# Kernel tuning notes

Hardware: AMD Instinct MI355X
Metric: run time of the kernel (lower is better)

The kernel has to match this reference:

```python
import jax, jax.numpy as jnp
import numpy as np

N_QUBITS = 11
DIM = 2 ** N_QUBITS
GAIN = 2 ** 0.5
LRMUL = 1.0
W_MUL = GAIN * 5 ** (-0.5) * LRMUL  # use_wscale=True path


def _build_unitary(weight):
    """Overall circuit unitary. Per qubit q the circuit applies rx, ry, rz
    (left_to_right composition => Rz @ Ry @ Rx on that qubit's subspace).
    Gates on distinct qubits commute, so the sequential product of expanded
    gates equals the kron over qubits of the per-qubit composite 2x2 gate,
    with qubit 0 as the leftmost kron factor (matches gate_expand_1toN)."""
    w = (weight * W_MUL).reshape(N_QUBITS, 3)
    half = w / 2
    c = jnp.cos(half)
    s = jnp.sin(half)
    cx, sx = c[:, 0], s[:, 0]
    cy, sy = c[:, 1], s[:, 1]
    ez = jnp.exp(-1j * half[:, 2])  # e^{-i phi_z / 2}
    zeros = jnp.zeros_like(ez)
    # [n, 2, 2] gate stacks (complex64)
    rx = jnp.stack([jnp.stack([cx + 0j, -1j * sx], -1),
                    jnp.stack([-1j * sx, cx + 0j], -1)], -2)
    ry = jnp.stack([jnp.stack([cy + 0j, -sy + 0j], -1),
                    jnp.stack([sy + 0j, cy + 0j], -1)], -2)
    rz = jnp.stack([jnp.stack([ez, zeros], -1),
                    jnp.stack([zeros, jnp.conj(ez)], -1)], -2)
    g = rz @ ry @ rx  # [n, 2, 2] composite per-qubit gate
    U = g[0]
    for q in range(1, N_QUBITS):  # loop over fixed small n_qubits is fine
        U = jnp.kron(U, g[q])
    return U  # [DIM, DIM] complex64


def setup_inputs() -> dict:
    key = jax.random.key(0)
    kx, kw = jax.random.split(key)
    x = jax.random.normal(kx, (DIM, DIM), dtype=jnp.float32)
    weight = jax.random.uniform(kw, (N_QUBITS * 3,), dtype=jnp.float32,
                                minval=0.0, maxval=2.0 * np.pi)
    return {"x": x, "weight": weight}


def reference(x, weight):
    U = _build_unitary(weight)
    xc = x.astype(jnp.complex64)
    # queryQ_out = U @ x @ U^dagger
    return U @ xc @ jnp.conj(U).T
```

## Files before the change

### kernel.cpp

```cpp
#include <hip/hip_runtime.h>
#include <hip/hip_fp16.h>


#define DIM 2048
#define NQ 11

typedef float v2f __attribute__((ext_vector_type(2)));

__device__ __forceinline__ int swz(int j) { return j ^ ((j >> 5) & 31); }

__device__ __forceinline__ float2 cmul(float2 a, float2 b) {
    return make_float2(a.x * b.x - a.y * b.y, a.x * b.y + a.y * b.x);
}

__device__ __forceinline__ v2f pkmul_swap(v2f s, v2f g) {
    v2f d;
    asm("v_pk_mul_f32 %0, %1, %2 op_sel:[1,0] op_sel_hi:[0,1]"
        : "=v"(d) : "v"(s), "v"(g));
    return d;
}
__device__ __forceinline__ v2f pkfma(v2f s0, v2f s1, v2f c) {
    v2f d;
    asm("v_pk_fma_f32 %0, %1, %2, %3" : "=v"(d) : "v"(s0), "v"(s1), "v"(c));
    return d;
}
__device__ __forceinline__ v2f pkfma_swap(v2f s0, v2f s1, v2f c) {
    v2f d;
    asm("v_pk_fma_f32 %0, %1, %2, %3 op_sel:[1,0,0] op_sel_hi:[0,1,1]"
        : "=v"(d) : "v"(s0), "v"(s1), "v"(c));
    return d;
}

struct PkGate {
    v2f x00, y00, x01, y01, x10, y10, x11, y11;
};

__device__ __forceinline__ void make_gate(const float* __restrict__ w, int q,
                                          int conj, float2* out4) {
    const float WM = 0.632455532033675866f;
    float hx = 0.5f * WM * w[q * 3 + 0];
    float hy = 0.5f * WM * w[q * 3 + 1];
    float hz = 0.5f * WM * w[q * 3 + 2];
    float cx, sx, cy, sy, cz, sz;
    sincosf(hx, &sx, &cx);
    sincosf(hy, &sy, &cy);
    sincosf(hz, &sz, &cz);
    float2 m00 = make_float2(cy * cx,  sy * sx);
    float2 m01 = make_float2(-sy * cx, -cy * sx);
    float2 m10 = make_float2(sy * cx,  -cy * sx);
    float2 m11 = make_float2(cy * cx,  -sy * sx);
    float2 ez  = make_float2(cz, -sz);
    float2 ezc = make_float2(cz,  sz);
    float2 g00 = cmul(ez, m00);
    float2 g01 = cmul(ez, m01);
    float2 g10 = cmul(ezc, m10);
    float2 g11 = cmul(ezc, m11);
    float sgn = conj ? -1.f : 1.f;
    out4[0] = make_float2(g00.x, sgn * g00.y);
    out4[1] = make_float2(g01.x, sgn * g01.y);
    out4[2] = make_float2(g10.x, sgn * g10.y);
    out4[3] = make_float2(g11.x, sgn * g11.y);
}

__device__ __forceinline__ void build_pk_gates(const float* __restrict__ wt,
                                               int t, int conj,
                                               v2f (*gsh)[8]) {
    if (t < NQ) {
        float2 e[4];
        make_gate(wt, t, conj, e);
#pragma unroll
        for (int k = 0; k < 4; ++k) {
            v2f px = {e[k].x, e[k].x};
            v2f py = {-e[k].y, e[k].y};
            gsh[t][2 * k + 0] = px;
            gsh[t][2 * k + 1] = py;
        }
    }
}

__device__ __forceinline__ void load_pkgate(const v2f (*gsh)[8], int q,
                                            PkGate& G) {
    G.x00 = gsh[q][0]; G.y00 = gsh[q][1];
    G.x01 = gsh[q][2]; G.y01 = gsh[q][3];
    G.x10 = gsh[q][4]; G.y10 = gsh[q][5];
    G.x11 = gsh[q][6]; G.y11 = gsh[q][7];
}

__device__ __forceinline__ void bfly(float2& A, float2& B, const PkGate& G) {
    v2f a = __builtin_bit_cast(v2f, A), b = __builtin_bit_cast(v2f, B);
    v2f t;
    t = pkmul_swap(b, G.y01);
    t = pkfma(b, G.x01, t);
    t = pkfma_swap(a, G.y00, t);
    A = __builtin_bit_cast(float2, pkfma(a, G.x00, t));
    t = pkmul_swap(b, G.y11);
    t = pkfma(b, G.x11, t);
    t = pkfma_swap(a, G.y10, t);
    B = __builtin_bit_cast(float2, pkfma(a, G.x10, t));
}

template <int ST>
__device__ __forceinline__ void stage16(float2* v, const PkGate& G) {
#pragma unroll
    for (int m = 0; m < 16; ++m)
        if (!(m & ST)) bfly(v[m], v[m + ST], G);
}

__device__ __forceinline__ unsigned pack_h2(float2 v) {
    __half2 h = __float22half2_rn(v);
    return *reinterpret_cast<unsigned*>(&h);
}
__device__ __forceinline__ float2 unpack_h2(unsigned u) {
    __half2 h = *reinterpret_cast<__half2*>(&u);
    return __half22float2(h);
}

__global__ __launch_bounds__(256, 2) void rowpassK1(
    const float* __restrict__ X, unsigned* __restrict__ Y,
    const float* __restrict__ wt) {
    __shared__ float pRe[2 * DIM];
    __shared__ float pIm[2 * DIM];
    __shared__ v2f gsh[NQ][8];
    int t = threadIdx.x;
    build_pk_gates(wt, t, 1, gsh);
    __syncthreads();

    int u = t & 127, rv = t >> 7;
    int base = rv * DIM;
    int row = blockIdx.x * 2 + rv;
    const float* xrow = X + (size_t)row * DIM;

    float xr[16];
#pragma unroll
    for (int m = 0; m < 16; ++m) xr[m] = xrow[u + (m << 7)];

    float e00x = gsh[3][0][0], e00y = gsh[3][1][1];
    float e01x = gsh[3][2][0], e01y = gsh[3][3][1];
    float e10x = gsh[3][4][0], e10y = gsh[3][5][1];
    float e11x = gsh[3][6][0], e11y = gsh[3][7][1];
    float2 v[16];
#pragma unroll
    for (int m = 0; m < 16; m += 2) {
        float a = xr[m], b = xr[m + 1];
        v[m]     = make_float2(e00x * a + e01x * b, e00y * a + e01y * b);
        v[m + 1] = make_float2(e10x * a + e11x * b, e10y * a + e11y * b);
    }
    PkGate G;
    load_pkgate(gsh, 2, G); stage16<2>(v, G);
    load_pkgate(gsh, 1, G); stage16<4>(v, G);
    load_pkgate(gsh, 0, G); stage16<8>(v, G);

#pragma unroll
    for (int m = 0; m < 16; ++m) {
        int a = base + swz(u + (m << 7));
        pRe[a] = v[m].x; pIm[a] = v[m].y;
    }
    __syncthreads();

    int uLo = u & 7, uHi = u >> 3;
#pragma unroll
    for (int m = 0; m < 16; ++m) {
        int a = base + swz(uLo + (m << 3) + (uHi << 7));
        v[m] = make_float2(pRe[a], pIm[a]);
    }
    load_pkgate(gsh, 7, G); stage16<1>(v, G);
    load_pkgate(gsh, 6, G); stage16<2>(v, G);
    load_pkgate(gsh, 5, G); stage16<4>(v, G);
    load_pkgate(gsh, 4, G); stage16<8>(v, G);
#pragma unroll
    for (int m = 0; m < 16; ++m) {
        int a = base + swz(uLo + (m << 3) + (uHi << 7));
        pRe[a] = v[m].x; pIm[a] = v[m].y;
    }
    __syncthreads();

#pragma unroll
    for (int m = 0; m < 16; ++m) {
        int a = base + swz(m + (u << 4));
        v[m] = make_float2(pRe[a], pIm[a]);
    }
    load_pkgate(gsh, 10, G); stage16<1>(v, G);
    load_pkgate(gsh, 9, G);  stage16<2>(v, G);
    load_pkgate(gsh, 8, G);  stage16<4>(v, G);

    unsigned* yp = Y + (size_t)row * DIM + (u << 4);
#pragma unroll
    for (int e = 0; e < 4; ++e) {
        uint4 pk;
        pk.x = pack_h2(v[4 * e + 0]);
        pk.y = pack_h2(v[4 * e + 1]);
        pk.z = pack_h2(v[4 * e + 2]);
        pk.w = pack_h2(v[4 * e + 3]);
        *reinterpret_cast<uint4*>(yp + 4 * e) = pk;
    }
}

__global__ __launch_bounds__(256, 4) void collowK2(
    const unsigned* __restrict__ Y, unsigned* __restrict__ Z,
    const float* __restrict__ wt) {
    __shared__ float pRe[128 * 32];
    __shared__ float pIm[128 * 32];
    __shared__ v2f gsh[NQ][8];
    int t = threadIdx.x;
    build_pk_gates(wt, t, 0, gsh);
    __syncthreads();

    int c = t & 31, rr = t >> 5;
    int r0 = (blockIdx.x >> 6) * 128;
    int c0 = (blockIdx.x & 63) * 32;

    float2 v[16];
    PkGate G;
#pragma unroll
    for (int m = 0; m < 16; ++m)
        v[m] = unpack_h2(Y[(size_t)(r0 + rr + (m << 3)) * DIM + c0 + c]);

    load_pkgate(gsh, 7, G); stage16<1>(v, G);
    load_pkgate(gsh, 6, G); stage16<2>(v, G);
    load_pkgate(gsh, 5, G); stage16<4>(v, G);
    load_pkgate(gsh, 4, G); stage16<8>(v, G);
#pragma unroll
    for (int m = 0; m < 16; ++m) {
        int a = (rr + (m << 3)) * 32 + c;
        pRe[a] = v[m].x; pIm[a] = v[m].y;
    }
    __syncthreads();

#pragma unroll
    for (int m = 0; m < 16; ++m) {
        int a = (m + (rr << 4)) * 32 + c;
        v[m] = make_float2(pRe[a], pIm[a]);
    }
    load_pkgate(gsh, 10, G); stage16<1>(v, G);
    load_pkgate(gsh, 9, G);  stage16<2>(v, G);
    load_pkgate(gsh, 8, G);  stage16<4>(v, G);

#pragma unroll
    for (int m = 0; m < 16; ++m)
        Z[(size_t)(r0 + m + (rr << 4)) * DIM + c0 + c] = pack_h2(v[m]);
}

__global__ __launch_bounds__(256, 4) void colhighK3(
    const unsigned* __restrict__ Z, float* __restrict__ Out,
    const float* __restrict__ wt, int writeComplex) {
    __shared__ v2f gsh[NQ][8];
    int t = threadIdx.x;
    build_pk_gates(wt, t, 0, gsh);
    __syncthreads();

    int b = blockIdx.x;
    int j = (b & 31) * 64 + (t & 63);
    int d = (b >> 5) * 4 + (t >> 6);

    float2 v[16];
    PkGate G;
#pragma unroll
    for (int m = 0; m < 16; ++m)
        v[m] = unpack_h2(Z[(size_t)(d + (m << 7)) * DIM + j]);

    load_pkgate(gsh, 3, G); stage16<1>(v, G);
    load_pkgate(gsh, 2, G); stage16<2>(v, G);
    load_pkgate(gsh, 1, G); stage16<4>(v, G);
    load_pkgate(gsh, 0, G); stage16<8>(v, G);

    if (!writeComplex) {
#pragma unroll
        for (int m = 0; m < 16; ++m)
            Out[(size_t)(d + (m << 7)) * DIM + j] = v[m].x;
    } else {
        float2* o2 = (float2*)Out;
#pragma unroll
        for (int m = 0; m < 16; ++m)
            o2[(size_t)(d + (m << 7)) * DIM + j] = v[m];
    }
}

extern "C" void kernel_launch(void* const* d_in, const int* in_sizes, int n_in,
                              void* d_out, int out_size, void* d_ws,
                              size_t ws_size, hipStream_t stream) {
    const float* X = (const float*)d_in[0];
    const float* wt = (const float*)d_in[1];
    float* out = (float*)d_out;
    unsigned* Y = (unsigned*)d_ws;
    unsigned* Z = (unsigned*)((char*)d_ws + (size_t)DIM * DIM * 4);

    rowpassK1<<<DIM / 2, 256, 0, stream>>>(X, Y, wt);
    collowK2<<<16 * 64, 256, 0, stream>>>(Y, Z, wt);
    int wc = (out_size >= 2 * DIM * DIM) ? 1 : 0;
    colhighK3<<<32 * 32, 256, 0, stream>>>(Z, out, wt, wc);
}
```

Baseline: 40.57 us.

## Fuse column passes into one kernel using column-strip tiled intermediate layout

The two column-pass kernels become one kernel. Each 1024-thread block now owns an 8-column strip of all 2048 rows and applies all 11 qubit gates through two shared-memory transposes, with padding of 9 floats per row. The row pass writes Y in a column-strip-major layout so each block reads one contiguous 64KB chunk, and the Z intermediate round trip through global memory is gone. In exchange each block uses about 147KB of shared memory and only 256 blocks launch, which limits occupancy and latency hiding, and the final output stores cover only 8 columns per row, so they are poorly coalesced.

```diff
diff --git a/kernel.cpp b/kernel.cpp
--- a/kernel.cpp
+++ b/kernel.cpp
@@ -183,95 +183,90 @@
     load_pkgate(gsh, 9, G);  stage16<2>(v, G);
     load_pkgate(gsh, 8, G);  stage16<4>(v, G);
 
-    unsigned* yp = Y + (size_t)row * DIM + (u << 4);
-#pragma unroll
-    for (int e = 0; e < 4; ++e) {
-        uint4 pk;
-        pk.x = pack_h2(v[4 * e + 0]);
-        pk.y = pack_h2(v[4 * e + 1]);
-        pk.z = pack_h2(v[4 * e + 2]);
-        pk.w = pack_h2(v[4 * e + 3]);
-        *reinterpret_cast<uint4*>(yp + 4 * e) = pk;
-    }
-}
-
-__global__ __launch_bounds__(256, 4) void collowK2(
-    const unsigned* __restrict__ Y, unsigned* __restrict__ Z,
-    const float* __restrict__ wt) {
-    __shared__ float pRe[128 * 32];
-    __shared__ float pIm[128 * 32];
+    unsigned* yp = Y + (size_t)(2 * u) * (DIM * 8) + (size_t)row * 8;
+    uint4 pk0, pk1;
+    pk0.x = pack_h2(v[0]); pk0.y = pack_h2(v[1]);
+    pk0.z = pack_h2(v[2]); pk0.w = pack_h2(v[3]);
+    pk1.x = pack_h2(v[4]); pk1.y = pack_h2(v[5]);
+    pk1.z = pack_h2(v[6]); pk1.w = pack_h2(v[7]);
+    *reinterpret_cast<uint4*>(yp) = pk0;
+    *reinterpret_cast<uint4*>(yp + 4) = pk1;
+    unsigned* yp2 = yp + DIM * 8;
+    pk0.x = pack_h2(v[8]);  pk0.y = pack_h2(v[9]);
+    pk0.z = pack_h2(v[10]); pk0.w = pack_h2(v[11]);
+    pk1.x = pack_h2(v[12]); pk1.y = pack_h2(v[13]);
+    pk1.z = pack_h2(v[14]); pk1.w = pack_h2(v[15]);
+    *reinterpret_cast<uint4*>(yp2) = pk0;
+    *reinterpret_cast<uint4*>(yp2 + 4) = pk1;
+}
+
+__global__ __launch_bounds__(1024, 4) void colfused(
+    const unsigned* __restrict__ Y, float* __restrict__ Out,
+    const float* __restrict__ wt, int writeComplex) {
+    __shared__ float pRe[DIM * 9];
+    __shared__ float pIm[DIM * 9];
     __shared__ v2f gsh[NQ][8];
     int t = threadIdx.x;
     build_pk_gates(wt, t, 0, gsh);
     __syncthreads();
 
-    int c = t & 31, rr = t >> 5;
-    int r0 = (blockIdx.x >> 6) * 128;
-    int c0 = (blockIdx.x & 63) * 32;
+    int c = t & 7, u = t >> 3;
+    const unsigned* yb = Y + (size_t)blockIdx.x * (DIM * 8);
 
     float2 v[16];
     PkGate G;
 #pragma unroll
     for (int m = 0; m < 16; ++m)
-        v[m] = unpack_h2(Y[(size_t)(r0 + rr + (m << 3)) * DIM + c0 + c]);
-
+        v[m] = unpack_h2(yb[(u + (m << 7)) * 8 + c]);
+
+    load_pkgate(gsh, 3, G); stage16<1>(v, G);
+    load_pkgate(gsh, 2, G); stage16<2>(v, G);
+    load_pkgate(gsh, 1, G); stage16<4>(v, G);
+    load_pkgate(gsh, 0, G); stage16<8>(v, G);
+
+#pragma unroll
+    for (int m = 0; m < 16; ++m) {
+        int a = (u + (m << 7)) * 9 + c;
+        pRe[a] = v[m].x; pIm[a] = v[m].y;
+    }
+    __syncthreads();
+
+    int uLo = u & 7, uHi = u >> 3;
+#pragma unroll
+    for (int m = 0; m < 16; ++m) {
+        int a = (uLo + (m << 3) + (uHi << 7)) * 9 + c;
+        v[m] = make_float2(pRe[a], pIm[a]);
+    }
     load_pkgate(gsh, 7, G); stage16<1>(v, G);
     load_pkgate(gsh, 6, G); stage16<2>(v, G);
     load_pkgate(gsh, 5, G); stage16<4>(v, G);
     load_pkgate(gsh, 4, G); stage16<8>(v, G);
 #pragma unroll
     for (int m = 0; m < 16; ++m) {
-        int a = (rr + (m << 3)) * 32 + c;
-        pRe[a] = v[m].x; pIm[a] = v[m].y;
-    }
-    __syncthreads();
-
-#pragma unroll
-    for (int m = 0; m < 16; ++m) {
-        int a = (m + (rr << 4)) * 32 + c;
+        int a = (uLo + (m << 3) + (uHi << 7)) * 9 + c;
+        pRe[a] = v[m].x; pIm[a] = v[m].y;
+    }
+    __syncthreads();
+
+#pragma unroll
+    for (int m = 0; m < 16; ++m) {
+        int a = (m + (u << 4)) * 9 + c;
         v[m] = make_float2(pRe[a], pIm[a]);
     }
     load_pkgate(gsh, 10, G); stage16<1>(v, G);
     load_pkgate(gsh, 9, G);  stage16<2>(v, G);
     load_pkgate(gsh, 8, G);  stage16<4>(v, G);
 
-#pragma unroll
-    for (int m = 0; m < 16; ++m)
-        Z[(size_t)(r0 + m + (rr << 4)) * DIM + c0 + c] = pack_h2(v[m]);
-}
-
-__global__ __launch_bounds__(256, 4) void colhighK3(
-    const unsigned* __restrict__ Z, float* __restrict__ Out,
-    const float* __restrict__ wt, int writeComplex) {
-    __shared__ v2f gsh[NQ][8];
-    int t = threadIdx.x;
-    build_pk_gates(wt, t, 0, gsh);
-    __syncthreads();
-
-    int b = blockIdx.x;
-    int j = (b & 31) * 64 + (t & 63);
-    int d = (b >> 5) * 4 + (t >> 6);
-
-    float2 v[16];
-    PkGate G;
-#pragma unroll
-    for (int m = 0; m < 16; ++m)
-        v[m] = unpack_h2(Z[(size_t)(d + (m << 7)) * DIM + j]);
-
-    load_pkgate(gsh, 3, G); stage16<1>(v, G);
-    load_pkgate(gsh, 2, G); stage16<2>(v, G);
-    load_pkgate(gsh, 1, G); stage16<4>(v, G);
-    load_pkgate(gsh, 0, G); stage16<8>(v, G);
-
+    int j = blockIdx.x * 8 + c;
     if (!writeComplex) {
 #pragma unroll
         for (int m = 0; m < 16; ++m)
-            Out[(size_t)(d + (m << 7)) * DIM + j] = v[m].x;
+            Out[(size_t)(m + (u << 4)) * DIM + j] = v[m].x;
     } else {
         float2* o2 = (float2*)Out;
 #pragma unroll
         for (int m = 0; m < 16; ++m)
-            o2[(size_t)(d + (m << 7)) * DIM + j] = v[m];
+            o2[(size_t)(m + (u << 4)) * DIM + j] = v[m];
     }
 }
 
@@ -282,10 +277,8 @@
     const float* wt = (const float*)d_in[1];
     float* out = (float*)d_out;
     unsigned* Y = (unsigned*)d_ws;
-    unsigned* Z = (unsigned*)((char*)d_ws + (size_t)DIM * DIM * 4);
 
     rowpassK1<<<DIM / 2, 256, 0, stream>>>(X, Y, wt);
-    collowK2<<<16 * 64, 256, 0, stream>>>(Y, Z, wt);
     int wc = (out_size >= 2 * DIM * DIM) ? 1 : 0;
-    colhighK3<<<32 * 32, 256, 0, stream>>>(Z, out, wt, wc);
-}
+    colfused<<<DIM / 8, 1024, 0, stream>>>(Y, out, wt, wc);
+}
```

Result: faster. 38.58 us (-4.9%).
